# Performance work log

Hardware: AMD Instinct MI355X
Metric: run time of the kernel (lower is better)

## Reference

```python
import jax, jax.numpy as jnp
import numpy as np

D, H, DFF, MD = 1024, 16, 4096, 128
B, TS, TT = 8, 512, 512
EPS = 1e-6


def _ln(x, s, b):
    m = jnp.mean(x, axis=-1, keepdims=True)
    v = jnp.mean((x - m) ** 2, axis=-1, keepdims=True)
    return (x - m) * jax.lax.rsqrt(v + EPS) * s + b


def _rel_bias(emb, qlen, klen):
    # T5-style bidirectional bucket: [H, qlen, klen]
    q = jnp.arange(qlen)[:, None]
    k = jnp.arange(klen)[None, :]
    rp = k - q
    bucket = jnp.where(rp < 0, jnp.minimum(-rp, MD - 1), jnp.minimum(rp, MD - 1) + MD)
    return emb[bucket].transpose(2, 0, 1)


def _mha(xq, xkv, w_in, b_in, w_out, b_out, bias):
    # nn.MultiheadAttention math: packed in_proj [3D,D], additive attn bias [H,Tq,Tk]
    Bq, Tq, _ = xq.shape
    Tk = xkv.shape[1]
    hd = D // H
    wq, wk, wv = jnp.split(w_in, 3, axis=0)
    bq, bk, bv = jnp.split(b_in, 3, axis=0)
    q = (xq @ wq.T + bq).reshape(Bq, Tq, H, hd).transpose(0, 2, 1, 3)
    k = (xkv @ wk.T + bk).reshape(Bq, Tk, H, hd).transpose(0, 2, 1, 3)
    v = (xkv @ wv.T + bv).reshape(Bq, Tk, H, hd).transpose(0, 2, 1, 3)
    scores = jnp.einsum('bhqd,bhkd->bhqk', q, k) / jnp.sqrt(jnp.asarray(hd, xq.dtype))
    scores = scores + bias[None]
    attn = jax.nn.softmax(scores, axis=-1)
    out = jnp.einsum('bhqk,bhkd->bhqd', attn, v)
    out = out.transpose(0, 2, 1, 3).reshape(Bq, Tq, D)
    return out @ w_out.T + b_out


def setup_inputs() -> dict:
    key = jax.random.key(0)
    ks = jax.random.split(key, 40)
    std = 0.02

    def n(i, shape):
        return jax.random.normal(ks[i], shape, dtype=jnp.float32) * std

    return {
        'src': jax.random.normal(ks[0], (B, TS, D), dtype=jnp.float32),
        'tgt': jax.random.normal(ks[1], (B, TT, D), dtype=jnp.float32),
        # encoder layer
        'enc_in_w': n(2, (3 * D, D)), 'enc_in_b': jnp.zeros((3 * D,)),
        'enc_out_w': n(3, (D, D)), 'enc_out_b': jnp.zeros((D,)),
        'enc_ff1_w': n(4, (DFF, D)), 'enc_ff1_b': jnp.zeros((DFF,)),
        'enc_ff2_w': n(5, (D, DFF)), 'enc_ff2_b': jnp.zeros((D,)),
        'enc_n1_s': jnp.ones((D,)), 'enc_n1_b': jnp.zeros((D,)),
        'enc_n2_s': jnp.ones((D,)), 'enc_n2_b': jnp.zeros((D,)),
        'enc_rel': n(6, (2 * MD, H)),
        # decoder layer
        'dec_sa_in_w': n(7, (3 * D, D)), 'dec_sa_in_b': jnp.zeros((3 * D,)),
        'dec_sa_out_w': n(8, (D, D)), 'dec_sa_out_b': jnp.zeros((D,)),
        'dec_ca_in_w': n(9, (3 * D, D)), 'dec_ca_in_b': jnp.zeros((3 * D,)),
        'dec_ca_out_w': n(10, (D, D)), 'dec_ca_out_b': jnp.zeros((D,)),
        'dec_ff1_w': n(11, (DFF, D)), 'dec_ff1_b': jnp.zeros((DFF,)),
        'dec_ff2_w': n(12, (D, DFF)), 'dec_ff2_b': jnp.zeros((D,)),
        'dec_n1_s': jnp.ones((D,)), 'dec_n1_b': jnp.zeros((D,)),
        'dec_n2_s': jnp.ones((D,)), 'dec_n2_b': jnp.zeros((D,)),
        'dec_n3_s': jnp.ones((D,)), 'dec_n3_b': jnp.zeros((D,)),
        'dec_rel_self': n(13, (2 * MD, H)),
        'dec_rel_cross': n(14, (2 * MD, H)),
    }


def reference(src, tgt,
              enc_in_w, enc_in_b, enc_out_w, enc_out_b,
              enc_ff1_w, enc_ff1_b, enc_ff2_w, enc_ff2_b,
              enc_n1_s, enc_n1_b, enc_n2_s, enc_n2_b, enc_rel,
              dec_sa_in_w, dec_sa_in_b, dec_sa_out_w, dec_sa_out_b,
              dec_ca_in_w, dec_ca_in_b, dec_ca_out_w, dec_ca_out_b,
              dec_ff1_w, dec_ff1_b, dec_ff2_w, dec_ff2_b,
              dec_n1_s, dec_n1_b, dec_n2_s, dec_n2_b, dec_n3_s, dec_n3_b,
              dec_rel_self, dec_rel_cross):
    Ts, Tt = src.shape[1], tgt.shape[1]

    # ---- encoder layer (pre-LN) ----
    eb = _rel_bias(enc_rel, Ts, Ts)  # [H,Ts,Ts]
    x = src
    x = x + _mha(_ln(x, enc_n1_s, enc_n1_b), _ln(x, enc_n1_s, enc_n1_b),
                 enc_in_w, enc_in_b, enc_out_w, enc_out_b, eb)
    h = _ln(x, enc_n2_s, enc_n2_b)
    x = x + (jax.nn.relu(h @ enc_ff1_w.T + enc_ff1_b) @ enc_ff2_w.T + enc_ff2_b)
    memory = x

    # ---- decoder layer (pre-LN) ----
    causal = jnp.where(jnp.arange(Tt)[None, :] > jnp.arange(Tt)[:, None], -jnp.inf, 0.0)
    sb = _rel_bias(dec_rel_self, Tt, Tt) + causal[None]  # [H,Tt,Tt]
    cb = _rel_bias(dec_rel_cross, Tt, Ts)                # [H,Tt,Ts]
    y = tgt
    yn = _ln(y, dec_n1_s, dec_n1_b)
    y = y + _mha(yn, yn, dec_sa_in_w, dec_sa_in_b, dec_sa_out_w, dec_sa_out_b, sb)
    y = y + _mha(_ln(y, dec_n2_s, dec_n2_b), memory,
                 dec_ca_in_w, dec_ca_in_b, dec_ca_out_w, dec_ca_out_b, cb)
    h = _ln(y, dec_n3_s, dec_n3_b)
    y = y + (jax.nn.relu(h @ dec_ff1_w.T + dec_ff1_b) @ dec_ff2_w.T + dec_ff2_b)
    return y
```

## Files before the change

kernel.cpp:

```cpp
#include <hip/hip_runtime.h>

using u16 = unsigned short;

typedef float f32x4 __attribute__((ext_vector_type(4)));
typedef __bf16 bf16x8v __attribute__((ext_vector_type(8)));
typedef bf16x8v bf16x8 __attribute__((may_alias));
typedef u16 u16x8v __attribute__((ext_vector_type(8)));
typedef u16x8v u16x8 __attribute__((may_alias));
typedef u16 u16x4v __attribute__((ext_vector_type(4)));
typedef u16x4v u16x4 __attribute__((may_alias));
typedef float f32x4v __attribute__((ext_vector_type(4)));
typedef f32x4v float4a __attribute__((may_alias));

#define GPTR(p) ((__attribute__((address_space(1))) void*)(p))
#define LPTR(p) ((__attribute__((address_space(3))) void*)(p))

__device__ __forceinline__ u16 f2bf(float f) {
  unsigned u = __builtin_bit_cast(unsigned, f);
  u += 0x7FFFu + ((u >> 16) & 1u);
  return (u16)(u >> 16);
}

__device__ __forceinline__ f32x4 mfma16(bf16x8 a, bf16x8 b, f32x4 c) {
  return __builtin_amdgcn_mfma_f32_16x16x32_bf16(a, b, c, 0, 0, 0);
}

struct Srcs { const float* s[10]; };

__global__ __launch_bounds__(256) void cvt_all(Srcs srcs, u16* __restrict__ dst) {
  constexpr int off[11] = {0, 786432, 1048576, 2097152, 3145728,
                           3932160, 4194304, 4980736, 5242880, 6291456, 7340032};
  const int i = blockIdx.x * 256 + threadIdx.x;
  int r = 0;
#pragma unroll
  for (int j = 1; j < 10; j++) r += (i >= off[j]);
  float4a v = ((const float4a*)srcs.s[r])[i - off[r]];
  u16x4 o;
  o[0] = f2bf(v[0]); o[1] = f2bf(v[1]); o[2] = f2bf(v[2]); o[3] = f2bf(v[3]);
  ((u16x4*)dst)[i] = o;
}

__global__ __launch_bounds__(256) void add_cvt(const float* __restrict__ a,
                                               const float* __restrict__ b,
                                               u16* __restrict__ o) {
  const int i = blockIdx.x * 256 + threadIdx.x;
  float4a va = ((const float4a*)a)[i];
  float4a vb = ((const float4a*)b)[i];
  u16x4 ov;
#pragma unroll
  for (int j = 0; j < 4; j++) ov[j] = f2bf(va[j] + vb[j]);
  ((u16x4*)o)[i] = ov;
}

__global__ __launch_bounds__(256) void add_f32(float* __restrict__ o,
                                               const float* __restrict__ b) {
  const int i = blockIdx.x * 256 + threadIdx.x;
  float4a vo = ((float4a*)o)[i];
  float4a vb = ((const float4a*)b)[i];
#pragma unroll
  for (int j = 0; j < 4; j++) vo[j] += vb[j];
  ((float4a*)o)[i] = vo;
}

__global__ __launch_bounds__(256) void ln_k(const float* __restrict__ x,
                                            const float* __restrict__ sc,
                                            const float* __restrict__ bi,
                                            u16* __restrict__ out) {
  const int row = blockIdx.x, tid = threadIdx.x;
  float4a v = ((const float4a*)(x + (size_t)row * 1024))[tid];
  float s1 = v[0] + v[1] + v[2] + v[3];
  float s2 = v[0]*v[0] + v[1]*v[1] + v[2]*v[2] + v[3]*v[3];
#pragma unroll
  for (int off = 32; off; off >>= 1) { s1 += __shfl_xor(s1, off); s2 += __shfl_xor(s2, off); }
  __shared__ float red[8];
  if ((tid & 63) == 0) { red[tid >> 6] = s1; red[4 + (tid >> 6)] = s2; }
  __syncthreads();
  s1 = red[0] + red[1] + red[2] + red[3];
  s2 = red[4] + red[5] + red[6] + red[7];
  const float mean = s1 * (1.f / 1024.f);
  const float rstd = rsqrtf(s2 * (1.f / 1024.f) - mean * mean + 1e-6f);
  float4a s4 = ((const float4a*)sc)[tid];
  float4a b4 = ((const float4a*)bi)[tid];
  u16x4 o;
#pragma unroll
  for (int j = 0; j < 4; j++) o[j] = f2bf((v[j] - mean) * rstd * s4[j] + b4[j]);
  ((u16x4*)(out + (size_t)row * 1024))[tid] = o;
}

template <int BN_T, int MW, int EPI, int PF>
__global__ __launch_bounds__(256) void gemm_bt(
    const u16* __restrict__ A, int lda,
    const u16* __restrict__ W, int ldw,
    const float* __restrict__ bias,
    const float* __restrict__ C0, int ldc0,
    void* __restrict__ outv, int ldo, int K,
    float* __restrict__ part) {
  constexpr int BM = 128, BK = 64;
  constexpr int NW = 4 / MW;
  constexpr int FM = BM / MW / 16;
  constexpr int FN = BN_T / NW / 16;
  constexpr int RA = (BM * BK * 2) / 4096;
  constexpr int RB = (BN_T * BK * 2) / 4096;
  constexpr int NB = PF ? 2 : 1;
  __shared__ alignas(16) u16 As[NB][BM * BK];
  __shared__ alignas(16) u16 Bs[NB][BN_T * BK];
  const int tid = threadIdx.x, lane = tid & 63, wv = tid >> 6;
  const int kb = (EPI == 3) ? blockIdx.z * K : 0;

  const int gx = gridDim.x;
  const int nwg = gx * gridDim.y;
  const int orig = blockIdx.y * gx + blockIdx.x;
  const int qq = nwg >> 3, rr = nwg & 7;
  const int xcd = orig & 7, idx = orig >> 3;
  const int wg = (xcd < rr ? xcd * (qq + 1) : rr * (qq + 1) + (xcd - rr) * qq) + idx;
  const int bm = (wg / gx) * BM, bn = (wg % gx) * BN_T;

  const int wr = (wv / NW) * (BM / MW);
  const int wc = (wv % NW) * (BN_T / NW);
  const int la = lane & 15, lg = lane >> 4;
  const int r7 = la & 7;
  const int srow = wv * 8 + (lane >> 3);
  const int scol = ((lane & 7) ^ (lane >> 3)) << 3;
  const u16* gA = A + (size_t)(bm + srow) * lda + scol;
  const u16* gB = W + (size_t)(bn + srow) * ldw + scol;

  f32x4 acc[FM][FN] = {};

  auto stage = [&](int buf, int k0) {
#pragma unroll
    for (int r = 0; r < RA; r++)
      __builtin_amdgcn_global_load_lds(GPTR(gA + (size_t)r * 32 * lda + k0),
                                       LPTR(&As[buf][(wv * 8 + r * 32) * BK]), 16, 0, 0);
#pragma unroll
    for (int r = 0; r < RB; r++)
      __builtin_amdgcn_global_load_lds(GPTR(gB + (size_t)r * 32 * ldw + k0),
                                       LPTR(&Bs[buf][(wv * 8 + r * 32) * BK]), 16, 0, 0);
  };

  auto compute = [&](int buf) {
#pragma unroll
    for (int kk = 0; kk < BK; kk += 32) {
      const int off = ((((kk >> 3) + lg) ^ r7) << 3);
      bf16x8 af[FM], bfr[FN];
#pragma unroll
      for (int m = 0; m < FM; m++)
        af[m] = *(const bf16x8*)&As[buf][(wr + m * 16 + la) * BK + off];
#pragma unroll
      for (int n = 0; n < FN; n++)
        bfr[n] = *(const bf16x8*)&Bs[buf][(wc + n * 16 + la) * BK + off];
#pragma unroll
      for (int m = 0; m < FM; m++)
#pragma unroll
        for (int n = 0; n < FN; n++)
          acc[m][n] = mfma16(af[m], bfr[n], acc[m][n]);
    }
  };

  if constexpr (PF) {
    stage(0, kb);
    int buf = 0;
    const int NT = K / BK;
    for (int t = 0; t < NT; ++t) {
      if (t + 1 < NT) {
        stage(buf ^ 1, kb + (t + 1) * BK);
        if constexpr (RA + RB == 8)
          asm volatile("s_waitcnt vmcnt(8)" ::: "memory");
        else
          asm volatile("s_waitcnt vmcnt(6)" ::: "memory");
      } else {
        asm volatile("s_waitcnt vmcnt(0)" ::: "memory");
      }
      __builtin_amdgcn_s_barrier();
      __builtin_amdgcn_sched_barrier(0);
      compute(buf);
      __builtin_amdgcn_s_barrier();
      buf ^= 1;
    }
  } else {
    for (int k0 = 0; k0 < K; k0 += BK) {
      __syncthreads();
      stage(0, kb + k0);
      __syncthreads();
      compute(0);
    }
  }

  const bool addb = (EPI != 3) || (blockIdx.z == 0);
  float bv[FN];
#pragma unroll
  for (int n = 0; n < FN; n++) bv[n] = addb ? bias[bn + wc + n * 16 + la] : 0.f;
#pragma unroll
  for (int m = 0; m < FM; m++) {
#pragma unroll
    for (int j = 0; j < 4; j++) {
      const int row = bm + wr + m * 16 + (lane >> 4) * 4 + j;
#pragma unroll
      for (int n = 0; n < FN; n++) {
        const int col = bn + wc + n * 16 + la;
        float v = acc[m][n][j] + bv[n];
        if constexpr (EPI == 1) v = fmaxf(v, 0.f);
        if constexpr (EPI == 2) {
          ((float*)outv)[(size_t)row * ldo + col] = v + C0[(size_t)row * ldc0 + col];
        } else if constexpr (EPI == 3) {
          if (blockIdx.z == 0)
            ((float*)outv)[(size_t)row * ldo + col] = v + C0[(size_t)row * ldc0 + col];
          else
            part[(size_t)row * ldo + col] = v;
        } else {
          ((u16*)outv)[(size_t)row * ldo + col] = f2bf(v);
        }
      }
    }
  }
}

template <bool CAUSAL>
__global__ __launch_bounds__(256) void attn_k(
    const u16* __restrict__ Qb, int ldq,
    const u16* __restrict__ Kb, int ldk,
    const u16* __restrict__ Vb, int ldv,
    const float* __restrict__ rel,
    u16* __restrict__ Ob, int ldo,
    int Tq, int Tk) {
  __shared__ alignas(16) u16 Ks[128][72];
  __shared__ alignas(16) u16 Vt[64][136];
  __shared__ alignas(16) u16 Ps[4][16][136];
  __shared__ float biasl[256];
  const int tid = threadIdx.x, lane = tid & 63, w = tid >> 6;
  const int b = blockIdx.y >> 4, h = blockIdx.y & 15;
  const int q0 = blockIdx.x * 64;
  const int la = lane & 15, lg = lane >> 4;

  biasl[tid] = rel[tid * 16 + h];

  const int qr0 = q0 + w * 16;
  const u16* qp = Qb + (size_t)(b * Tq + qr0 + la) * ldq + h * 64 + lg * 8;
  const bf16x8 qf0 = *(const bf16x8*)qp;
  const bf16x8 qf1 = *(const bf16x8*)(qp + 32);

  float m[4], sm[4];
  f32x4 acc[4] = {};
#pragma unroll
  for (int j = 0; j < 4; j++) { m[j] = -1e30f; sm[j] = 0.f; }

  const int kv_end = CAUSAL ? (q0 + 64) : Tk;
  const int srow = tid >> 3, scol = (tid & 7) * 8;
  for (int kv0 = 0; kv0 < kv_end; kv0 += 128) {
    __syncthreads();
#pragma unroll
    for (int r = 0; r < 4; r++) {
      const int row = r * 32 + srow;
      const size_t gr = (size_t)(b * Tk + kv0 + row);
      *(u16x8*)&Ks[row][scol] = *(const u16x8*)&Kb[gr * ldk + h * 64 + scol];
      u16x8 vv = *(const u16x8*)&Vb[gr * ldv + h * 64 + scol];
#pragma unroll
      for (int j = 0; j < 8; j++) Vt[scol + j][row] = vv[j];
    }
    __syncthreads();

    f32x4 s[8];
#pragma unroll
    for (int kvt = 0; kvt < 8; kvt++) {
      const bf16x8 kf0 = *(const bf16x8*)&Ks[kvt * 16 + la][lg * 8];
      const bf16x8 kf1 = *(const bf16x8*)&Ks[kvt * 16 + la][32 + lg * 8];
      f32x4 t = {};
      t = mfma16(qf0, kf0, t);
      t = mfma16(qf1, kf1, t);
      const int kc = kv0 + kvt * 16 + la;
#pragma unroll
      for (int j = 0; j < 4; j++) {
        const int qr = qr0 + lg * 4 + j;
        const int rp = kc - qr;
        const int bucket = rp < 0 ? (rp > -127 ? -rp : 127) : (rp < 127 ? rp : 127) + 128;
        float sv = t[j] * 0.125f + biasl[bucket];
        if (CAUSAL && kc > qr) sv = -1e30f;
        s[kvt][j] = sv;
      }
    }
    float alpha[4];
#pragma unroll
    for (int j = 0; j < 4; j++) {
      float tm = s[0][j];
#pragma unroll
      for (int kvt = 1; kvt < 8; kvt++) tm = fmaxf(tm, s[kvt][j]);
#pragma unroll
      for (int off = 1; off < 16; off <<= 1) tm = fmaxf(tm, __shfl_xor(tm, off));
      const float mn = fmaxf(m[j], tm);
      alpha[j] = __expf(m[j] - mn);
      m[j] = mn;
      float r = 0.f;
#pragma unroll
      for (int kvt = 0; kvt < 8; kvt++) {
        const float p = __expf(s[kvt][j] - mn);
        s[kvt][j] = p;
        r += p;
      }
#pragma unroll
      for (int off = 1; off < 16; off <<= 1) r += __shfl_xor(r, off);
      sm[j] = sm[j] * alpha[j] + r;
    }
#pragma unroll
    for (int kvt = 0; kvt < 8; kvt++)
#pragma unroll
      for (int j = 0; j < 4; j++)
        Ps[w][lg * 4 + j][kvt * 16 + la] = f2bf(s[kvt][j]);
#pragma unroll
    for (int n = 0; n < 4; n++)
#pragma unroll
      for (int j = 0; j < 4; j++)
        acc[n][j] *= alpha[j];
#pragma unroll
    for (int kq = 0; kq < 4; kq++) {
      const bf16x8 pf = *(const bf16x8*)&Ps[w][la][kq * 32 + lg * 8];
#pragma unroll
      for (int n = 0; n < 4; n++) {
        const bf16x8 vf = *(const bf16x8*)&Vt[n * 16 + la][kq * 32 + lg * 8];
        acc[n] = mfma16(pf, vf, acc[n]);
      }
    }
  }
#pragma unroll
  for (int n = 0; n < 4; n++)
#pragma unroll
    for (int j = 0; j < 4; j++) {
      const int qr = qr0 + lg * 4 + j;
      Ob[(size_t)(b * Tq + qr) * ldo + h * 64 + n * 16 + la] = f2bf(acc[n][j] / sm[j]);
    }
}

extern "C" void kernel_launch(void* const* d_in, const int* in_sizes, int n_in,
                              void* d_out, int out_size, void* d_ws, size_t ws_size,
                              hipStream_t stream) {
  (void)in_sizes; (void)n_in; (void)out_size; (void)ws_size;
  const float* src       = (const float*)d_in[0];
  const float* tgt       = (const float*)d_in[1];
  const float* enc_in_w  = (const float*)d_in[2];
  const float* enc_in_b  = (const float*)d_in[3];
  const float* enc_out_w = (const float*)d_in[4];
  const float* enc_out_b = (const float*)d_in[5];
  const float* enc_ff1_w = (const float*)d_in[6];
  const float* enc_ff1_b = (const float*)d_in[7];
  const float* enc_ff2_w = (const float*)d_in[8];
  const float* enc_ff2_b = (const float*)d_in[9];
  const float* enc_n1_s  = (const float*)d_in[10];
  const float* enc_n1_b  = (const float*)d_in[11];
  const float* enc_n2_s  = (const float*)d_in[12];
  const float* enc_n2_b  = (const float*)d_in[13];
  const float* enc_rel   = (const float*)d_in[14];
  const float* dsa_in_w  = (const float*)d_in[15];
  const float* dsa_in_b  = (const float*)d_in[16];
  const float* dsa_out_w = (const float*)d_in[17];
  const float* dsa_out_b = (const float*)d_in[18];
  const float* dca_in_w  = (const float*)d_in[19];
  const float* dca_in_b  = (const float*)d_in[20];
  const float* dca_out_w = (const float*)d_in[21];
  const float* dca_out_b = (const float*)d_in[22];
  const float* dff1_w    = (const float*)d_in[23];
  const float* dff1_b    = (const float*)d_in[24];
  const float* dff2_w    = (const float*)d_in[25];
  const float* dff2_b    = (const float*)d_in[26];
  const float* dn1_s     = (const float*)d_in[27];
  const float* dn1_b     = (const float*)d_in[28];
  const float* dn2_s     = (const float*)d_in[29];
  const float* dn2_b     = (const float*)d_in[30];
  const float* dn3_s     = (const float*)d_in[31];
  const float* dn3_b     = (const float*)d_in[32];
  const float* drel_s    = (const float*)d_in[33];
  const float* drel_c    = (const float*)d_in[34];
  float* fo = (float*)d_out;

  char* w8 = (char*)d_ws;
  float* x_ws  = (float*)(w8 + 0);
  u16* ln_buf  = (u16*)(w8 + 16777216);
  u16* qkv     = (u16*)(w8 + 25165824);
  u16* attn_o  = (u16*)(w8 + 50331648);
  u16* ffh     = qkv;
  u16* memb    = (u16*)(w8 + 58720256);
  u16* wb      = (u16*)(w8 + 67108864);

  u16* w_enc_in  = wb;
  u16* w_enc_out = wb + 3145728;
  u16* w_enc_f1  = wb + 4194304;
  u16* w_enc_f2  = wb + 8388608;
  u16* w_dsa_in  = wb + 12582912;
  u16* w_dsa_out = wb + 15728640;
  u16* w_dca_in  = wb + 16777216;
  u16* w_dca_out = wb + 19922944;
  u16* w_dff1    = wb + 20971520;
  u16* w_dff2    = wb + 25165824;

  Srcs srcs = {{enc_in_w, enc_out_w, enc_ff1_w, enc_ff2_w, dsa_in_w,
                dsa_out_w, dca_in_w, dca_out_w, dff1_w, dff2_w}};
  cvt_all<<<dim3(28672), 256, 0, stream>>>(srcs, wb);

  ln_k<<<dim3(4096), 256, 0, stream>>>(src, enc_n1_s, enc_n1_b, ln_buf);
  gemm_bt<128,2,0,0><<<dim3(24, 32), 256, 0, stream>>>(ln_buf, 1024, w_enc_in, 1024, enc_in_b, nullptr, 0, qkv, 3072, 1024, nullptr);
  attn_k<false><<<dim3(8, 128), 256, 0, stream>>>(qkv, 3072, qkv + 1024, 3072, qkv + 2048, 3072, enc_rel, attn_o, 1024, 512, 512);
  gemm_bt<64,4,2,1><<<dim3(16, 32), 256, 0, stream>>>(attn_o, 1024, w_enc_out, 1024, enc_out_b, src, 1024, x_ws, 1024, 1024, nullptr);
  ln_k<<<dim3(4096), 256, 0, stream>>>(x_ws, enc_n2_s, enc_n2_b, ln_buf);
  gemm_bt<128,2,1,0><<<dim3(32, 32), 256, 0, stream>>>(ln_buf, 1024, w_enc_f1, 1024, enc_ff1_b, nullptr, 0, ffh, 4096, 1024, nullptr);
  gemm_bt<128,2,3,1><<<dim3(8, 32, 2), 256, 0, stream>>>(ffh, 4096, w_enc_f2, 4096, enc_ff2_b, x_ws, 1024, x_ws, 1024, 2048, fo);
  add_cvt<<<dim3(4096), 256, 0, stream>>>(x_ws, fo, memb);

  ln_k<<<dim3(4096), 256, 0, stream>>>(tgt, dn1_s, dn1_b, ln_buf);
  gemm_bt<128,2,0,0><<<dim3(24, 32), 256, 0, stream>>>(ln_buf, 1024, w_dsa_in, 1024, dsa_in_b, nullptr, 0, qkv, 3072, 1024, nullptr);
  attn_k<true><<<dim3(8, 128), 256, 0, stream>>>(qkv, 3072, qkv + 1024, 3072, qkv + 2048, 3072, drel_s, attn_o, 1024, 512, 512);
  gemm_bt<64,4,2,1><<<dim3(16, 32), 256, 0, stream>>>(attn_o, 1024, w_dsa_out, 1024, dsa_out_b, tgt, 1024, fo, 1024, 1024, nullptr);

  ln_k<<<dim3(4096), 256, 0, stream>>>(fo, dn2_s, dn2_b, ln_buf);
  gemm_bt<64,4,0,1><<<dim3(16, 32), 256, 0, stream>>>(ln_buf, 1024, w_dca_in, 1024, dca_in_b, nullptr, 0, qkv, 3072, 1024, nullptr);
  gemm_bt<128,2,0,0><<<dim3(16, 32), 256, 0, stream>>>(memb, 1024, w_dca_in + 1048576, 1024, dca_in_b + 1024, nullptr, 0, qkv + 1024, 3072, 1024, nullptr);
  attn_k<false><<<dim3(8, 128), 256, 0, stream>>>(qkv, 3072, qkv + 1024, 3072, qkv + 2048, 3072, drel_c, attn_o, 1024, 512, 512);
  gemm_bt<64,4,2,1><<<dim3(16, 32), 256, 0, stream>>>(attn_o, 1024, w_dca_out, 1024, dca_out_b, fo, 1024, fo, 1024, 1024, nullptr);

  ln_k<<<dim3(4096), 256, 0, stream>>>(fo, dn3_s, dn3_b, ln_buf);
  gemm_bt<128,2,1,0><<<dim3(32, 32), 256, 0, stream>>>(ln_buf, 1024, w_dff1, 1024, dff1_b, nullptr, 0, ffh, 4096, 1024, nullptr);
  gemm_bt<128,2,3,1><<<dim3(8, 32, 2), 256, 0, stream>>>(ffh, 4096, w_dff2, 4096, dff2_b, fo, 1024, fo, 1024, 2048, x_ws);
  add_f32<<<dim3(4096), 256, 0, stream>>>(fo, x_ws);
}
```

Measured before the change: 613.0 us.

## Load K directly into LDS with XOR swizzles and alias P onto K buffer

The attention kernel now loads K tiles with global_load_lds straight into an unpadded, XOR-swizzled LDS layout instead of staging them through registers. V is still transposed through registers, but now into a swizzled layout. The per-wave P staging buffer is placed in the K tile region behind an extra barrier, which cuts LDS use and may allow more resident blocks. The intent is lower load latency, fewer LDS bank conflicts and higher occupancy, at the cost of one more __syncthreads per KV tile.

Result: slower. 682.7 us, median of 2 (+11.4%).

```diff
diff --git a/kernel.cpp b/kernel.cpp
--- a/kernel.cpp
+++ b/kernel.cpp
@@ -222,14 +222,13 @@
     const float* __restrict__ rel,
     u16* __restrict__ Ob, int ldo,
     int Tq, int Tk) {
-  __shared__ alignas(16) u16 Ks[128][72];
-  __shared__ alignas(16) u16 Vt[64][136];
-  __shared__ alignas(16) u16 Ps[4][16][136];
+  __shared__ alignas(16) u16 Ks[128 * 64];
+  __shared__ alignas(16) u16 Vt[64 * 136];
   __shared__ float biasl[256];
   const int tid = threadIdx.x, lane = tid & 63, w = tid >> 6;
   const int b = blockIdx.y >> 4, h = blockIdx.y & 15;
   const int q0 = blockIdx.x * 64;
-  const int la = lane & 15, lg = lane >> 4;
+  const int la = lane & 15, lg = lane >> 4, r7 = la & 7;
 
   biasl[tid] = rel[tid * 16 + h];
 
@@ -244,35 +243,47 @@
   for (int j = 0; j < 4; j++) { m[j] = -1e30f; sm[j] = 0.f; }
 
   const int kv_end = CAUSAL ? (q0 + 64) : Tk;
-  const int srow = tid >> 3, scol = (tid & 7) * 8;
+  const int scolK = ((lane & 7) ^ (lane >> 3)) << 3;
+  const u16* gK = Kb + (size_t)(b * Tk + w * 8 + (lane >> 3)) * ldk + h * 64 + scolK;
+  const int vrow = tid >> 3;
+  const int vcol = (tid & 7) * 8;
+  const int vsw = (tid & 3) * 8;
+  const u16* gV = Vb + (size_t)(b * Tk + vrow) * ldv + h * 64 + vcol;
+  u16* Pw = Ks + w * 2048;
+
   for (int kv0 = 0; kv0 < kv_end; kv0 += 128) {
     __syncthreads();
 #pragma unroll
+    for (int r = 0; r < 4; r++)
+      __builtin_amdgcn_global_load_lds(GPTR(gK + (size_t)(kv0 + r * 32) * ldk),
+                                       LPTR(&Ks[(w * 8 + r * 32) * 64]), 16, 0, 0);
+    u16x8 vreg[4];
+#pragma unroll
+    for (int r = 0; r < 4; r++)
+      vreg[r] = *(const u16x8*)(gV + (size_t)(kv0 + r * 32) * ldv);
+    __syncthreads();
+#pragma unroll
     for (int r = 0; r < 4; r++) {
-      const int row = r * 32 + srow;
-      const size_t gr = (size_t)(b * Tk + kv0 + row);
-      *(u16x8*)&Ks[row][scol] = *(const u16x8*)&Kb[gr * ldk + h * 64 + scol];
-      u16x8 vv = *(const u16x8*)&Vb[gr * ldv + h * 64 + scol];
-#pragma unroll
-      for (int j = 0; j < 8; j++) Vt[scol + j][row] = vv[j];
-    }
-    __syncthreads();
+      const int rsw = (r * 32 + vrow) ^ vsw;
+#pragma unroll
+      for (int j = 0; j < 8; j++) Vt[(vcol + j) * 136 + rsw] = vreg[r][j];
+    }
 
     f32x4 s[8];
 #pragma unroll
     for (int kvt = 0; kvt < 8; kvt++) {
-      const bf16x8 kf0 = *(const bf16x8*)&Ks[kvt * 16 + la][lg * 8];
-      const bf16x8 kf1 = *(const bf16x8*)&Ks[kvt * 16 + la][32 + lg * 8];
-      f32x4 t = {};
-      t = mfma16(qf0, kf0, t);
-      t = mfma16(qf1, kf1, t);
+      const bf16x8 kf0 = *(const bf16x8*)&Ks[(kvt * 16 + la) * 64 + ((lg ^ r7) << 3)];
+      const bf16x8 kf1 = *(const bf16x8*)&Ks[(kvt * 16 + la) * 64 + (((4 + lg) ^ r7) << 3)];
+      f32x4 t2 = {};
+      t2 = mfma16(qf0, kf0, t2);
+      t2 = mfma16(qf1, kf1, t2);
       const int kc = kv0 + kvt * 16 + la;
 #pragma unroll
       for (int j = 0; j < 4; j++) {
         const int qr = qr0 + lg * 4 + j;
         const int rp = kc - qr;
         const int bucket = rp < 0 ? (rp > -127 ? -rp : 127) : (rp < 127 ? rp : 127) + 128;
-        float sv = t[j] * 0.125f + biasl[bucket];
+        float sv = t2[j] * 0.125f + biasl[bucket];
         if (CAUSAL && kc > qr) sv = -1e30f;
         s[kvt][j] = sv;
       }
@@ -299,11 +310,16 @@
       for (int off = 1; off < 16; off <<= 1) r += __shfl_xor(r, off);
       sm[j] = sm[j] * alpha[j] + r;
     }
+    __syncthreads();
+
 #pragma unroll
     for (int kvt = 0; kvt < 8; kvt++)
 #pragma unroll
-      for (int j = 0; j < 4; j++)
-        Ps[w][lg * 4 + j][kvt * 16 + la] = f2bf(s[kvt][j]);
+      for (int j = 0; j < 4; j++) {
+        const int row = lg * 4 + j;
+        const int pb = ((kvt * 2 + (la >> 3)) ^ (row & 7)) << 3;
+        Pw[row * 128 + pb + (la & 7)] = f2bf(s[kvt][j]);
+      }
 #pragma unroll
     for (int n = 0; n < 4; n++)
 #pragma unroll
@@ -311,10 +327,12 @@
         acc[n][j] *= alpha[j];
 #pragma unroll
     for (int kq = 0; kq < 4; kq++) {
-      const bf16x8 pf = *(const bf16x8*)&Ps[w][la][kq * 32 + lg * 8];
+      const bf16x8 pf = *(const bf16x8*)&Pw[la * 128 + (((kq * 4 + lg) ^ r7) << 3)];
 #pragma unroll
       for (int n = 0; n < 4; n++) {
-        const bf16x8 vf = *(const bf16x8*)&Vt[n * 16 + la][kq * 32 + lg * 8];
+        const int dd = n * 16 + la;
+        const int cc = (kq * 32 + lg * 8) ^ (((dd >> 3) & 3) * 8);
+        const bf16x8 vf = *(const bf16x8*)&Vt[dd * 136 + cc];
         acc[n] = mfma16(pf, vf, acc[n]);
       }
     }
```
